# Optimization experiments

Hardware: AMD Instinct MI355X
Metric: run time of the kernel (lower is better)

Reference implementation:

```python
import jax, jax.numpy as jnp
import numpy as np

C = 19          # EEG channels
NP = C * C      # 361 channel pairs
D = 256         # UNIFIED_FEATURE_DIM
H = 8           # num_heads
HD = D // H     # head dim


def _build_mask():
    # rel[p, q] = True iff key-pair q shares a channel with query-pair p
    idx = np.arange(NP)
    ci, cj = idx // C, idx % C
    rel = ((ci[:, None] == ci[None, :]) | (ci[:, None] == cj[None, :]) |
           (cj[:, None] == ci[None, :]) | (cj[:, None] == cj[None, :]))
    return jnp.asarray(rel.reshape(C, C, NP))  # (channel_i, j, key_pair)

MASK = _build_mask()


def setup_inputs() -> dict:
    key = jax.random.key(0)
    ks = jax.random.split(key, 6)
    s = 0.05
    return {
        "x": jax.random.normal(ks[0], (32, NP, D), jnp.float32),
        # 19 stacked nn.MultiheadAttention modules: in_proj (3D, D) = [Wq; Wk; Wv]
        "w_in": jax.random.normal(ks[1], (C, 3 * D, D), jnp.float32) * s,
        "b_in": jnp.zeros((C, 3 * D), jnp.float32),
        "w_out": jax.random.normal(ks[2], (C, D, D), jnp.float32) * s,
        "b_out": jnp.zeros((C, D), jnp.float32),
        # fusion: nn.Linear(D, D)
        "w_fuse": jax.random.normal(ks[3], (D, D), jnp.float32) * s,
        "b_fuse": jnp.zeros((D,), jnp.float32),
    }


def reference(x, w_in, b_in, w_out, b_out, w_fuse, b_fuse):
    # x: (B, 361, D). Pair p=(i,j) at index i*19+j uses attention module i,
    # query = x[:, p], keys/values = pairs sharing channel i or j (mask).
    B = x.shape[0]
    wq, wk, wv = w_in[:, :D], w_in[:, D:2 * D], w_in[:, 2 * D:]
    bq, bk, bv = b_in[:, :D], b_in[:, D:2 * D], b_in[:, 2 * D:]

    # Per-channel K/V projections over all 361 pairs: (C, B, NP, D)
    K = jnp.einsum('bnd,ced->cbne', x, wk) + bk[:, None, None, :]
    V = jnp.einsum('bnd,ced->cbne', x, wv) + bv[:, None, None, :]
    # Queries grouped by first channel i: x reshaped to (B, C, C, D)
    xq = x.reshape(B, C, C, D)
    Q = jnp.einsum('bcjd,ced->cbje', xq, wq) + bq[:, None, None, :]  # (C,B,C,D)

    Qh = Q.reshape(C, B, C, H, HD)
    Kh = K.reshape(C, B, NP, H, HD)
    Vh = V.reshape(C, B, NP, H, HD)

    scale = 1.0 / jnp.sqrt(jnp.asarray(HD, x.dtype))
    scores = jnp.einsum('cbqhe,cbkhe->cbhqk', Qh, Kh) * scale  # (C,B,H,C,NP)
    scores = jnp.where(MASK[:, None, None, :, :], scores, -jnp.inf)
    attn = jax.nn.softmax(scores, axis=-1)

    out = jnp.einsum('cbhqk,cbkhe->cbqhe', attn, Vh).reshape(C, B, C, D)
    out = jnp.einsum('cbqd,ced->cbqe', out, w_out) + b_out[:, None, None, :]
    out = out.transpose(1, 0, 2, 3).reshape(B, NP, D)  # back to (B, 361, D)

    # fusion ('linear') + residual
    return out @ w_fuse.T + b_fuse + x
```

## Files before the change

### kernel.cpp

```cpp
#include <hip/hip_runtime.h>

#define CC 19
#define NPOS 361
#define NPAD 384
#define DIM 256
#define TKEY 32
#define NTILES 12

#define LDS_BYTES 70144

using bf16x8 = __attribute__((ext_vector_type(8))) short;
using f16x4  = __attribute__((ext_vector_type(4))) _Float16;
using floatx4 = __attribute__((ext_vector_type(4))) float;
using uintx2 = __attribute__((ext_vector_type(2))) unsigned int;

__device__ __forceinline__ unsigned short f2bf(float f) {
  unsigned u = __builtin_bit_cast(unsigned, f);
  u += 0x7fffu + ((u >> 16) & 1u);
  return (unsigned short)(u >> 16);
}

__device__ __forceinline__ f16x4 pack4h(float a, float b, float c2, float d) {
  const auto h01 = __builtin_amdgcn_cvt_pkrtz(a, b);
  const auto h23 = __builtin_amdgcn_cvt_pkrtz(c2, d);
  uintx2 uv = {__builtin_bit_cast(unsigned, h01), __builtin_bit_cast(unsigned, h23)};
  return __builtin_bit_cast(f16x4, uv);
}

__global__ void conv_all_kernel(const float* __restrict__ x,
                                const float* __restrict__ w_in,
                                const float* __restrict__ w_out,
                                const float* __restrict__ w_fuse,
                                unsigned short* __restrict__ ws) {
  const int j = blockIdx.x * 256 + threadIdx.x;
  float4 v = make_float4(0.f, 0.f, 0.f, 0.f);
  unsigned short* dst;
  if (j < 786432) {
    const int row = j >> 6;
    const int off = (j & 63) << 2;
    const int b = row / NPAD;
    const int r = row - b * NPAD;
    if (r < NPOS) v = *(const float4*)&x[(b * NPOS + r) * DIM + off];
    dst = &ws[row * DIM + off];
  } else if (j < 1720320) {
    const int k = j - 786432;
    v = *(const float4*)&w_in[k << 2];
    dst = &ws[3145728 + (k << 2)];
  } else if (j < 2031616) {
    const int k = j - 1720320;
    v = *(const float4*)&w_out[k << 2];
    dst = &ws[6881280 + (k << 2)];
  } else {
    const int k = j - 2031616;
    v = *(const float4*)&w_fuse[k << 2];
    dst = &ws[8126464 + (k << 2)];
  }
  ushort4 o;
  o.x = f2bf(v.x); o.y = f2bf(v.y); o.z = f2bf(v.z); o.w = f2bf(v.w);
  *(ushort4*)dst = o;
}

__launch_bounds__(512, 2)
__global__ void cgca_kernel(const float* __restrict__ xf,
                            const float* __restrict__ b_in,
                            const float* __restrict__ b_out,
                            const float* __restrict__ b_fuse,
                            const unsigned short* __restrict__ xbf,
                            const unsigned short* __restrict__ wibf,
                            const unsigned short* __restrict__ wobf,
                            const unsigned short* __restrict__ wfbf,
                            float* __restrict__ out) {
  const int bid = blockIdx.x;
  const int xcd = bid & 7;
  const int slot = bid >> 3;
  int c, b;
  if (slot < 64) {
    c = ((slot >> 5) << 3) + xcd;
    b = slot & 31;
  } else {
    const int widx = ((slot - 64) << 3) + xcd;
    c = 16 + (widx >> 5);
    b = widx & 31;
  }

  const int tid = threadIdx.x;
  const int w = tid >> 6;
  const int lane = tid & 63;
  const int quad = lane >> 4;
  const int l16 = lane & 15;
  const int eh = w * 32;

  extern __shared__ char smem[];
  unsigned short* sx = (unsigned short*)smem;
  unsigned* msk = (unsigned*)(smem + 67584);
  float* sL = (float*)(smem + 69120);
  unsigned short* bufx0 = sx;
  unsigned short* bufx1 = sx + 8448;

  const float scale = 0.25503486f;
  const floatx4 fzero = {0.f, 0.f, 0.f, 0.f};

  f16x4 qf[2][2];
  {
    bf16x8 wq[2][8];
#pragma unroll
    for (int m4 = 0; m4 < 2; ++m4)
#pragma unroll
      for (int k = 0; k < 8; ++k)
        wq[m4][k] = *(const bf16x8*)&wibf[(c * 768 + eh + m4 * 16 + l16) * DIM + k * 32 + quad * 8];
    float bq[2][4];
#pragma unroll
    for (int m4 = 0; m4 < 2; ++m4) {
      const float4 bv4 = *(const float4*)&b_in[c * 768 + eh + m4 * 16 + quad * 4];
      bq[m4][0] = bv4.x; bq[m4][1] = bv4.y; bq[m4][2] = bv4.z; bq[m4][3] = bv4.w;
    }
#pragma unroll
    for (int mt = 0; mt < 2; ++mt) {
      const int xrow = b * NPAD + c * CC + mt * 16 + l16;
      bf16x8 xq[8];
#pragma unroll
      for (int k = 0; k < 8; ++k)
        xq[k] = *(const bf16x8*)&xbf[xrow * DIM + k * 32 + quad * 8];
#pragma unroll
      for (int m4 = 0; m4 < 2; ++m4) {
        floatx4 acc = fzero;
#pragma unroll
        for (int k = 0; k < 8; ++k)
          acc = __builtin_amdgcn_mfma_f32_16x16x32_bf16(wq[m4][k], xq[k], acc, 0, 0, 0);
        qf[mt][m4] = pack4h((acc[0] + bq[m4][0]) * scale, (acc[1] + bq[m4][1]) * scale,
                            (acc[2] + bq[m4][2]) * scale, (acc[3] + bq[m4][3]) * scale);
      }
    }
  }

  bf16x8 wk[2][8], wv[2][8];
#pragma unroll
  for (int m4 = 0; m4 < 2; ++m4)
#pragma unroll
    for (int k = 0; k < 8; ++k) {
      wk[m4][k] =
          *(const bf16x8*)&wibf[(c * 768 + 256 + eh + m4 * 16 + l16) * DIM + k * 32 + quad * 8];
      wv[m4][k] =
          *(const bf16x8*)&wibf[(c * 768 + 512 + eh + m4 * 16 + l16) * DIM + k * 32 + quad * 8];
    }
  float bV[2];
#pragma unroll
  for (int ne = 0; ne < 2; ++ne) bV[ne] = b_in[c * 768 + 512 + eh + ne * 16 + l16];

  {
    const int q = tid >> 4;
    const int wd = tid & 15;
    if (wd < 12) {
      unsigned m = 0u;
      for (int i = 0; i < 32; ++i) {
        const int kabs = wd * 32 + i;
        const unsigned ki = ((unsigned)kabs * 110377u) >> 21;
        const unsigned kj = (unsigned)kabs - ki * 19u;
        if (kabs < NPOS && (ki == (unsigned)c || kj == (unsigned)c ||
                            ki == (unsigned)q || kj == (unsigned)q))
          m |= (1u << i);
      }
      msk[q * 12 + wd] = m;
    }
  }

#pragma unroll
  for (int u = 0; u < 2; ++u)
#pragma unroll
    for (int it = 0; it < 2; ++it) {
      const int cc2 = tid + it * 512;
      const int row = cc2 >> 5;
      const int col = (cc2 & 31) * 8;
      *(bf16x8*)&sx[u * 8448 + row * 264 + col] =
          *(const bf16x8*)&xbf[(b * NPAD + u * TKEY + row) * DIM + col];
    }

  floatx4 o_acc[2][2];
  float lsum[2] = {0.f, 0.f};
#pragma unroll
  for (int mt = 0; mt < 2; ++mt)
#pragma unroll
    for (int ne = 0; ne < 2; ++ne) o_acc[mt][ne] = fzero;

  __syncthreads();

  for (int s6 = 0; s6 < 6; ++s6) {
    const int tb = s6 * 2;
    if (s6 < 5) {
#pragma unroll
      for (int u = 0; u < 2; ++u) {
        const int t = tb + 2 + u;
        unsigned short* bxn = sx + (t & 3) * 8448;
#pragma unroll
        for (int it = 0; it < 2; ++it) {
          const int cc2 = tid + it * 512;
          const int row = cc2 >> 5;
          const int col = (cc2 & 31) * 8;
          *(bf16x8*)&bxn[row * 264 + col] =
              *(const bf16x8*)&xbf[(b * NPAD + t * TKEY + row) * DIM + col];
        }
      }
    }

#pragma unroll
    for (int u = 0; u < 2; ++u) {
      const int t = tb + u;
      const int t0 = t * TKEY;
      const unsigned short* bx = sx + (t & 3) * 8448;

      floatx4 aK[2][2], aV[2][2];
#pragma unroll
      for (int i = 0; i < 2; ++i)
#pragma unroll
        for (int j = 0; j < 2; ++j) { aK[i][j] = fzero; aV[i][j] = fzero; }
#pragma unroll
      for (int k = 0; k < 8; ++k) {
        bf16x8 xfr[2];
#pragma unroll
        for (int n4 = 0; n4 < 2; ++n4)
          xfr[n4] = *(const bf16x8*)&bx[(n4 * 16 + l16) * 264 + k * 32 + quad * 8];
#pragma unroll
        for (int m4 = 0; m4 < 2; ++m4)
#pragma unroll
          for (int n4 = 0; n4 < 2; ++n4) {
            aK[m4][n4] = __builtin_amdgcn_mfma_f32_16x16x32_bf16(wk[m4][k], xfr[n4], aK[m4][n4], 0, 0, 0);
            aV[n4][m4] = __builtin_amdgcn_mfma_f32_16x16x32_bf16(xfr[n4], wv[m4][k], aV[n4][m4], 0, 0, 0);
          }
      }

      f16x4 kf[2][2];
      f16x4 vf[2][2];
#pragma unroll
      for (int kt = 0; kt < 2; ++kt)
#pragma unroll
        for (int ec = 0; ec < 2; ++ec) {
          kf[kt][ec] = pack4h(aK[ec][kt][0], aK[ec][kt][1], aK[ec][kt][2], aK[ec][kt][3]);
          vf[kt][ec] = pack4h(aV[kt][ec][0], aV[kt][ec][1], aV[kt][ec][2], aV[kt][ec][3]);
        }

#pragma unroll
      for (int mt = 0; mt < 2; ++mt) {
        const int q = mt * 16 + l16;
        const unsigned mw = msk[q * 12 + t];
        f16x4 pf[2];
#pragma unroll
        for (int kt = 0; kt < 2; ++kt) {
          floatx4 s2 = __builtin_amdgcn_mfma_f32_16x16x16f16(kf[kt][0], qf[mt][0], fzero, 0, 0, 0);
          s2 = __builtin_amdgcn_mfma_f32_16x16x16f16(kf[kt][1], qf[mt][1], s2, 0, 0, 0);
          const unsigned mk = mw >> (kt * 16 + quad * 4);
          float p[4];
#pragma unroll
          for (int r = 0; r < 4; ++r)
            p[r] = (mk & (1u << r)) ? __builtin_exp2f(s2[r]) : 0.f;
          lsum[mt] += (p[0] + p[1]) + (p[2] + p[3]);
          pf[kt] = pack4h(p[0], p[1], p[2], p[3]);
        }
#pragma unroll
        for (int kt = 0; kt < 2; ++kt)
#pragma unroll
          for (int ne = 0; ne < 2; ++ne)
            o_acc[mt][ne] =
                __builtin_amdgcn_mfma_f32_16x16x16f16(pf[kt], vf[kt][ne], o_acc[mt][ne], 0, 0, 0);
      }
      (void)t0;
    }
    __syncthreads();
  }

#pragma unroll
  for (int mt = 0; mt < 2; ++mt) {
    lsum[mt] += __shfl_xor(lsum[mt], 16);
    lsum[mt] += __shfl_xor(lsum[mt], 32);
  }
  if (lane < 16) {
    sL[w * 32 + lane] = lsum[0];
    sL[w * 32 + 16 + lane] = lsum[1];
  }
  float invl[2][4];
#pragma unroll
  for (int mt = 0; mt < 2; ++mt)
#pragma unroll
    for (int r = 0; r < 4; ++r)
      invl[mt][r] = 1.f / sL[w * 32 + mt * 16 + quad * 4 + r];

#pragma unroll
  for (int mt = 0; mt < 2; ++mt)
#pragma unroll
    for (int ne = 0; ne < 2; ++ne)
#pragma unroll
      for (int r = 0; r < 4; ++r)
        bufx0[(mt * 16 + quad * 4 + r) * 264 + eh + ne * 16 + l16] =
            f2bf(o_acc[mt][ne][r] * invl[mt][r] + bV[ne]);
  __syncthreads();

#pragma unroll
  for (int mt = 0; mt < 2; ++mt) {
    bf16x8 a8[8];
#pragma unroll
    for (int k = 0; k < 8; ++k)
      a8[k] = *(const bf16x8*)&bufx0[(mt * 16 + l16) * 264 + k * 32 + quad * 8];
#pragma unroll
    for (int nt2 = 0; nt2 < 2; ++nt2) {
      const int e0 = w * 32 + nt2 * 16;
      floatx4 acc = fzero;
#pragma unroll
      for (int k = 0; k < 8; ++k) {
        bf16x8 b8 = *(const bf16x8*)&wobf[(c * 256 + e0 + l16) * DIM + k * 32 + quad * 8];
        acc = __builtin_amdgcn_mfma_f32_16x16x32_bf16(a8[k], b8, acc, 0, 0, 0);
      }
      const float bias = b_out[c * 256 + e0 + l16];
#pragma unroll
      for (int r = 0; r < 4; ++r)
        bufx1[(mt * 16 + quad * 4 + r) * 264 + e0 + l16] = f2bf(acc[r] + bias);
    }
  }
  __syncthreads();

#pragma unroll
  for (int mt = 0; mt < 2; ++mt) {
    bf16x8 a8[8];
#pragma unroll
    for (int k = 0; k < 8; ++k)
      a8[k] = *(const bf16x8*)&bufx1[(mt * 16 + l16) * 264 + k * 32 + quad * 8];
#pragma unroll
    for (int nt2 = 0; nt2 < 2; ++nt2) {
      const int e0 = w * 32 + nt2 * 16;
      floatx4 acc = fzero;
#pragma unroll
      for (int k = 0; k < 8; ++k) {
        bf16x8 b8 = *(const bf16x8*)&wfbf[(e0 + l16) * DIM + k * 32 + quad * 8];
        acc = __builtin_amdgcn_mfma_f32_16x16x32_bf16(a8[k], b8, acc, 0, 0, 0);
      }
      const float bfu = b_fuse[e0 + l16];
#pragma unroll
      for (int r = 0; r < 4; ++r) {
        const int row = mt * 16 + quad * 4 + r;
        if (row < CC) {
          const int gp = (b * NPOS + c * CC + row) * DIM + e0 + l16;
          out[gp] = acc[r] + bfu + xf[gp];
        }
      }
    }
  }
}

extern "C" void kernel_launch(void* const* d_in, const int* in_sizes, int n_in,
                              void* d_out, int out_size, void* d_ws, size_t ws_size,
                              hipStream_t stream) {
  const float* x      = (const float*)d_in[0];
  const float* w_in   = (const float*)d_in[1];
  const float* b_in   = (const float*)d_in[2];
  const float* w_out  = (const float*)d_in[3];
  const float* b_out  = (const float*)d_in[4];
  const float* w_fuse = (const float*)d_in[5];
  const float* b_fuse = (const float*)d_in[6];
  float* out = (float*)d_out;

  if (ws_size < (size_t)16384000) return;

  unsigned short* ws = (unsigned short*)d_ws;
  unsigned short* x_bf  = ws;
  unsigned short* wi_bf = ws + 3145728;
  unsigned short* wo_bf = ws + 6881280;
  unsigned short* wf_bf = ws + 8126464;

  conv_all_kernel<<<8000, 256, 0, stream>>>(x, w_in, w_out, w_fuse, ws);

  (void)hipFuncSetAttribute((const void*)cgca_kernel,
                            hipFuncAttributeMaxDynamicSharedMemorySize, LDS_BYTES);
  cgca_kernel<<<608, 512, LDS_BYTES, stream>>>(x, b_in, b_out, b_fuse, x_bf, wi_bf,
                                               wo_bf, wf_bf, out);
}
```

Baseline: 249.1 us.

## Split attention across head halves and move projection epilogue to separate kernel

The fused kernel is split in two. The attention kernel now runs 256-thread blocks, each covering half of the heads, so it launches twice as many blocks. It writes the normalized bf16 attention output into the output buffer as scratch. A second epilogue kernel reads that scratch back and applies the out-projection, the fusion linear layer and the residual. This aims to improve occupancy and load balance across CUs, at the cost of recomputing the K/V projection once per head half, an extra launch, and a global round trip for the intermediate.

Result: no change. 244.4 us (-1.9%).

```diff
diff --git a/kernel.cpp b/kernel.cpp
--- a/kernel.cpp
+++ b/kernel.cpp
@@ -7,7 +7,7 @@
 #define TKEY 32
 #define NTILES 12
 
-#define LDS_BYTES 70144
+#define LDS_BYTES 69632
 
 using bf16x8 = __attribute__((ext_vector_type(8))) short;
 using f16x4  = __attribute__((ext_vector_type(4))) _Float16;
@@ -60,42 +60,30 @@
   *(ushort4*)dst = o;
 }
 
-__launch_bounds__(512, 2)
-__global__ void cgca_kernel(const float* __restrict__ xf,
-                            const float* __restrict__ b_in,
-                            const float* __restrict__ b_out,
-                            const float* __restrict__ b_fuse,
+__launch_bounds__(256, 2)
+__global__ void attn_kernel(const float* __restrict__ b_in,
                             const unsigned short* __restrict__ xbf,
                             const unsigned short* __restrict__ wibf,
-                            const unsigned short* __restrict__ wobf,
-                            const unsigned short* __restrict__ wfbf,
                             float* __restrict__ out) {
   const int bid = blockIdx.x;
   const int xcd = bid & 7;
   const int slot = bid >> 3;
-  int c, b;
-  if (slot < 64) {
-    c = ((slot >> 5) << 3) + xcd;
-    b = slot & 31;
-  } else {
-    const int widx = ((slot - 64) << 3) + xcd;
-    c = 16 + (widx >> 5);
-    b = widx & 31;
-  }
+  const int c = slot >> 3;
+  const int p = ((slot & 7) << 3) | xcd;
+  const int b = p >> 1;
+  const int hb = p & 1;
 
   const int tid = threadIdx.x;
   const int w = tid >> 6;
   const int lane = tid & 63;
   const int quad = lane >> 4;
   const int l16 = lane & 15;
-  const int eh = w * 32;
+  const int eh = (hb * 4 + w) * 32;
 
   extern __shared__ char smem[];
   unsigned short* sx = (unsigned short*)smem;
   unsigned* msk = (unsigned*)(smem + 67584);
   float* sL = (float*)(smem + 69120);
-  unsigned short* bufx0 = sx;
-  unsigned short* bufx1 = sx + 8448;
 
   const float scale = 0.25503486f;
   const floatx4 fzero = {0.f, 0.f, 0.f, 0.f};
@@ -147,28 +135,26 @@
 #pragma unroll
   for (int ne = 0; ne < 2; ++ne) bV[ne] = b_in[c * 768 + 512 + eh + ne * 16 + l16];
 
-  {
-    const int q = tid >> 4;
-    const int wd = tid & 15;
-    if (wd < 12) {
-      unsigned m = 0u;
-      for (int i = 0; i < 32; ++i) {
-        const int kabs = wd * 32 + i;
-        const unsigned ki = ((unsigned)kabs * 110377u) >> 21;
-        const unsigned kj = (unsigned)kabs - ki * 19u;
-        if (kabs < NPOS && (ki == (unsigned)c || kj == (unsigned)c ||
-                            ki == (unsigned)q || kj == (unsigned)q))
-          m |= (1u << i);
-      }
-      msk[q * 12 + wd] = m;
-    }
+  for (int e2 = tid; e2 < 384; e2 += 256) {
+    const int q = e2 / 12;
+    const int wd = e2 - q * 12;
+    unsigned m = 0u;
+    for (int i = 0; i < 32; ++i) {
+      const int kabs = wd * 32 + i;
+      const unsigned ki = ((unsigned)kabs * 110377u) >> 21;
+      const unsigned kj = (unsigned)kabs - ki * 19u;
+      if (kabs < NPOS && (ki == (unsigned)c || kj == (unsigned)c ||
+                          ki == (unsigned)q || kj == (unsigned)q))
+        m |= (1u << i);
+    }
+    msk[e2] = m;
   }
 
 #pragma unroll
   for (int u = 0; u < 2; ++u)
 #pragma unroll
-    for (int it = 0; it < 2; ++it) {
-      const int cc2 = tid + it * 512;
+    for (int it = 0; it < 4; ++it) {
+      const int cc2 = tid + it * 256;
       const int row = cc2 >> 5;
       const int col = (cc2 & 31) * 8;
       *(bf16x8*)&sx[u * 8448 + row * 264 + col] =
@@ -192,8 +178,8 @@
         const int t = tb + 2 + u;
         unsigned short* bxn = sx + (t & 3) * 8448;
 #pragma unroll
-        for (int it = 0; it < 2; ++it) {
-          const int cc2 = tid + it * 512;
+        for (int it = 0; it < 4; ++it) {
+          const int cc2 = tid + it * 256;
           const int row = cc2 >> 5;
           const int col = (cc2 & 31) * 8;
           *(bf16x8*)&bxn[row * 264 + col] =
@@ -205,7 +191,6 @@
 #pragma unroll
     for (int u = 0; u < 2; ++u) {
       const int t = tb + u;
-      const int t0 = t * TKEY;
       const unsigned short* bx = sx + (t & 3) * 8448;
 
       floatx4 aK[2][2], aV[2][2];
@@ -262,9 +247,8 @@
             o_acc[mt][ne] =
                 __builtin_amdgcn_mfma_f32_16x16x16f16(pf[kt], vf[kt][ne], o_acc[mt][ne], 0, 0, 0);
       }
-      (void)t0;
-    }
-    __syncthreads();
+    }
+    if (s6 < 5) __syncthreads();
   }
 
 #pragma unroll
@@ -283,14 +267,56 @@
     for (int r = 0; r < 4; ++r)
       invl[mt][r] = 1.f / sL[w * 32 + mt * 16 + quad * 4 + r];
 
+  unsigned short* aop = (unsigned short*)(out + (size_t)(b * NPOS + c * CC) * DIM);
 #pragma unroll
   for (int mt = 0; mt < 2; ++mt)
 #pragma unroll
     for (int ne = 0; ne < 2; ++ne)
 #pragma unroll
-      for (int r = 0; r < 4; ++r)
-        bufx0[(mt * 16 + quad * 4 + r) * 264 + eh + ne * 16 + l16] =
-            f2bf(o_acc[mt][ne][r] * invl[mt][r] + bV[ne]);
+      for (int r = 0; r < 4; ++r) {
+        const int q = mt * 16 + quad * 4 + r;
+        if (q < CC)
+          aop[q * DIM + eh + ne * 16 + l16] =
+              f2bf(o_acc[mt][ne][r] * invl[mt][r] + bV[ne]);
+      }
+}
+
+__launch_bounds__(256)
+__global__ void epi_kernel(const float* __restrict__ xf,
+                           const float* __restrict__ b_out,
+                           const float* __restrict__ b_fuse,
+                           const unsigned short* __restrict__ wobf,
+                           const unsigned short* __restrict__ wfbf,
+                           float* __restrict__ out) {
+  const int bid = blockIdx.x;
+  const int xcd = bid & 7;
+  const int slot = bid >> 3;
+  const int c = slot >> 2;
+  const int b = ((slot & 3) << 3) | xcd;
+
+  const int tid = threadIdx.x;
+  const int w = tid >> 6;
+  const int lane = tid & 63;
+  const int quad = lane >> 4;
+  const int l16 = lane & 15;
+
+  __shared__ unsigned short sA[32 * 264];
+  __shared__ unsigned short sT[32 * 264];
+
+  const size_t fbase = (size_t)(b * NPOS + c * CC) * DIM;
+  const unsigned short* aop = (const unsigned short*)(out + fbase);
+  const floatx4 fzero = {0.f, 0.f, 0.f, 0.f};
+  const bf16x8 zero8 = {};
+
+#pragma unroll
+  for (int it = 0; it < 4; ++it) {
+    const int cc2 = tid + it * 256;
+    const int row = cc2 >> 5;
+    const int col = (cc2 & 31) * 8;
+    bf16x8 v = zero8;
+    if (row < CC) v = *(const bf16x8*)&aop[row * DIM + col];
+    *(bf16x8*)&sA[row * 264 + col] = v;
+  }
   __syncthreads();
 
 #pragma unroll
@@ -298,10 +324,10 @@
     bf16x8 a8[8];
 #pragma unroll
     for (int k = 0; k < 8; ++k)
-      a8[k] = *(const bf16x8*)&bufx0[(mt * 16 + l16) * 264 + k * 32 + quad * 8];
-#pragma unroll
-    for (int nt2 = 0; nt2 < 2; ++nt2) {
-      const int e0 = w * 32 + nt2 * 16;
+      a8[k] = *(const bf16x8*)&sA[(mt * 16 + l16) * 264 + k * 32 + quad * 8];
+#pragma unroll
+    for (int nt2 = 0; nt2 < 4; ++nt2) {
+      const int e0 = w * 64 + nt2 * 16;
       floatx4 acc = fzero;
 #pragma unroll
       for (int k = 0; k < 8; ++k) {
@@ -311,7 +337,7 @@
       const float bias = b_out[c * 256 + e0 + l16];
 #pragma unroll
       for (int r = 0; r < 4; ++r)
-        bufx1[(mt * 16 + quad * 4 + r) * 264 + e0 + l16] = f2bf(acc[r] + bias);
+        sT[(mt * 16 + quad * 4 + r) * 264 + e0 + l16] = f2bf(acc[r] + bias);
     }
   }
   __syncthreads();
@@ -321,10 +347,10 @@
     bf16x8 a8[8];
 #pragma unroll
     for (int k = 0; k < 8; ++k)
-      a8[k] = *(const bf16x8*)&bufx1[(mt * 16 + l16) * 264 + k * 32 + quad * 8];
-#pragma unroll
-    for (int nt2 = 0; nt2 < 2; ++nt2) {
-      const int e0 = w * 32 + nt2 * 16;
+      a8[k] = *(const bf16x8*)&sT[(mt * 16 + l16) * 264 + k * 32 + quad * 8];
+#pragma unroll
+    for (int nt2 = 0; nt2 < 4; ++nt2) {
+      const int e0 = w * 64 + nt2 * 16;
       floatx4 acc = fzero;
 #pragma unroll
       for (int k = 0; k < 8; ++k) {
@@ -336,7 +362,7 @@
       for (int r = 0; r < 4; ++r) {
         const int row = mt * 16 + quad * 4 + r;
         if (row < CC) {
-          const int gp = (b * NPOS + c * CC + row) * DIM + e0 + l16;
+          const size_t gp = fbase + (size_t)row * DIM + e0 + l16;
           out[gp] = acc[r] + bfu + xf[gp];
         }
       }
@@ -366,8 +392,9 @@
 
   conv_all_kernel<<<8000, 256, 0, stream>>>(x, w_in, w_out, w_fuse, ws);
 
-  (void)hipFuncSetAttribute((const void*)cgca_kernel,
+  (void)hipFuncSetAttribute((const void*)attn_kernel,
                             hipFuncAttributeMaxDynamicSharedMemorySize, LDS_BYTES);
-  cgca_kernel<<<608, 512, LDS_BYTES, stream>>>(x, b_in, b_out, b_fuse, x_bf, wi_bf,
-                                               wo_bf, wf_bf, out);
-}
+  attn_kernel<<<1216, 256, LDS_BYTES, stream>>>(b_in, x_bf, wi_bf, out);
+
+  epi_kernel<<<608, 256, 0, stream>>>(x, b_out, b_fuse, wo_bf, wf_bf, out);
+}
```
